# Performance work log

Hardware: AMD Instinct MI355X
Metric: run time of the kernel (lower is better)

Reference implementation:

```python
import jax, jax.numpy as jnp
import numpy as np

B, S, D_IN = 4, 2048, 512
H, D_OUT = 8, 64


def setup_inputs() -> dict:
    key = jax.random.key(0)
    k1, k2, k3 = jax.random.split(key, 3)
    x = jax.random.normal(k1, (B, S, D_IN), dtype=jnp.float32)
    # matches torch init: w ~ U(-0.8, 0.8), wo ~ U(-1, 1)
    w = jax.random.uniform(k2, (H, 3, D_IN, D_OUT), dtype=jnp.float32, minval=-0.8, maxval=0.8)
    wo = jax.random.uniform(k3, (H * D_OUT, D_OUT), dtype=jnp.float32, minval=-1.0, maxval=1.0)
    return {"x": x, "w": w, "wo": wo}


def reference(x, w, wo):
    d_out = w.shape[-1]
    # batched per-head projections: [B, H, S, D_OUT]
    q = jnp.einsum('bsi,hio->bhso', x, w[:, 0])
    k = jnp.einsum('bsi,hio->bhso', x, w[:, 1])
    v = jnp.einsum('bsi,hio->bhso', x, w[:, 2])
    scores = jnp.einsum('bhso,bhto->bhst', q, k) / jnp.sqrt(jnp.asarray(d_out, x.dtype))
    attn = jax.nn.softmax(scores, axis=-1)
    o = jnp.einsum('bhst,bhto->bhso', attn, v)  # [B, H, S, D_OUT]
    # concat heads along feature dim (head order matches torch cat order)
    o = jnp.transpose(o, (0, 2, 1, 3)).reshape(x.shape[0], x.shape[1], -1)
    return jnp.matmul(o, wo)
```

## Files before the change

### kernel.cpp

```cpp
#include <hip/hip_runtime.h>
#include <cstdint>
#include <cstddef>

#define S_LEN 2048
#define DIN   512
#define DOUT  64
#define NB    4
#define NH    8

typedef __attribute__((ext_vector_type(8))) short bf16x8;
typedef __attribute__((ext_vector_type(8))) _Float16 f16x8;
typedef __attribute__((ext_vector_type(4))) float f32x4;
typedef __attribute__((ext_vector_type(16))) float f32x16;

static __device__ __forceinline__ f32x4 mfma16(bf16x8 a, bf16x8 b, f32x4 c) {
    return __builtin_amdgcn_mfma_f32_16x16x32_bf16(a, b, c, 0, 0, 0);
}
static __device__ __forceinline__ f32x16 mfma32h(f16x8 a, f16x8 b, f32x16 c) {
    return __builtin_amdgcn_mfma_f32_32x32x16_f16(a, b, c, 0, 0, 0);
}

static __device__ __forceinline__ uint16_t f2bf(float x) {
    uint32_t u = __builtin_bit_cast(uint32_t, x);
    u += 0x7fffu + ((u >> 16) & 1u);
    return (uint16_t)(u >> 16);
}
static __device__ __forceinline__ float bf2f(uint16_t h) {
    uint32_t u = ((uint32_t)h) << 16;
    return __builtin_bit_cast(float, u);
}
static __device__ __forceinline__ uint32_t cvt_pk_bf16(float lo, float hi) {
    uint32_t r;
    asm("v_cvt_pk_bf16_f32 %0, %1, %2" : "=v"(r) : "v"(lo), "v"(hi));
    return r;
}
static __device__ __forceinline__ uint32_t cvt_pkrtz_f16(float lo, float hi) {
    return __builtin_bit_cast(uint32_t, __builtin_amdgcn_cvt_pkrtz(lo, hi));
}

typedef const __attribute__((address_space(1))) void* as1p;
typedef __attribute__((address_space(3))) void* as3p;
static __device__ __forceinline__ void gload_lds16(const void* g, void* l) {
    __builtin_amdgcn_global_load_lds((as1p)g, (as3p)l, 16, 0, 0);
}

__global__ __launch_bounds__(256) void prep_w(
    const float* __restrict__ w, const float* __restrict__ wo,
    uint16_t* __restrict__ whiT, uint16_t* __restrict__ wloT,
    uint16_t* __restrict__ woT)
{
    __shared__ float tile[64][65];
    const int blk = blockIdx.x;
    const int t = threadIdx.x;
    const int tq = t >> 6, tr = t & 63;

    if (blk < 192) {
        const int hp = blk >> 3, i0 = (blk & 7) * 64;
        const int p = hp % 3;
        const float s = (p == 0) ? 0.18033688011112042f : 1.0f;
        const float* __restrict__ src = w + (size_t)hp * (DIN * DOUT);
        #pragma unroll
        for (int r = 0; r < 16; ++r) {
            const int ir = r * 4 + tq;
            tile[ir][tr] = src[(size_t)(i0 + ir) * DOUT + tr];
        }
        __syncthreads();
        uint16_t* __restrict__ dh = whiT + (size_t)hp * (DOUT * DIN);
        uint16_t* __restrict__ dl = wloT + (size_t)hp * (DOUT * DIN);
        #pragma unroll
        for (int r = 0; r < 16; ++r) {
            const int o = r * 4 + tq;
            const float v = tile[tr][o] * s;
            const uint16_t hi = f2bf(v);
            dh[(size_t)o * DIN + i0 + tr] = hi;
            dl[(size_t)o * DIN + i0 + tr] = f2bf(v - bf2f(hi));
        }
    } else {
        const int i0 = (blk - 192) * 64;
        #pragma unroll
        for (int r = 0; r < 16; ++r) {
            const int ir = r * 4 + tq;
            tile[ir][tr] = wo[(size_t)(i0 + ir) * DOUT + tr];
        }
        __syncthreads();
        #pragma unroll
        for (int r = 0; r < 16; ++r) {
            const int o = r * 4 + tq;
            woT[(size_t)o * DIN + i0 + tr] = f2bf(tile[tr][o]);
        }
    }
}

__global__ __launch_bounds__(256) void split_x(
    const float* __restrict__ x, uint16_t* __restrict__ xhi, uint16_t* __restrict__ xlo)
{
    const size_t idx = ((size_t)blockIdx.x * 256 + threadIdx.x) * 8;
    const float4 a = *(const float4*)(x + idx);
    const float4 b = *(const float4*)(x + idx + 4);
    const float xv[8] = {a.x, a.y, a.z, a.w, b.x, b.y, b.z, b.w};
    union { uint16_t u[8]; uint4 v; } H, L;
    #pragma unroll
    for (int j = 0; j < 8; ++j) {
        const uint16_t hi = f2bf(xv[j]);
        H.u[j] = hi;
        L.u[j] = f2bf(xv[j] - bf2f(hi));
    }
    *(uint4*)(xhi + idx) = H.v;
    *(uint4*)(xlo + idx) = L.v;
}

__global__ __launch_bounds__(256, 2) void gemm_qkv(
    const uint16_t* __restrict__ xhi, const uint16_t* __restrict__ xlo,
    const uint16_t* __restrict__ whiT, const uint16_t* __restrict__ wloT,
    uint16_t* __restrict__ qf, uint16_t* __restrict__ kf,
    uint16_t* __restrict__ vT)
{
    __shared__ __align__(16) uint16_t lds[4 * 128 * 64];

    const int bid = blockIdx.x;
    const int xcd = bid & 7, wi = bid >> 3;
    const int mt = xcd * 8 + wi / 12, nt = wi % 12;
    const int m0 = mt * 128, n0 = nt * 128;
    const int tid = threadIdx.x;
    const int l = tid & 63, w = tid >> 6;
    const int g = l >> 4, lm = l & 15;
    const int wm = w >> 1, wn = w & 1;

    const f32x4 Z = {0.f, 0.f, 0.f, 0.f};
    f32x4 acc[4][4];
    #pragma unroll
    for (int a = 0; a < 4; ++a)
        #pragma unroll
        for (int b = 0; b < 4; ++b) acc[a][b] = Z;

    int srow[4], scol[4];
    #pragma unroll
    for (int i = 0; i < 4; ++i) {
        const int c = i * 256 + tid;
        srow[i] = c >> 3;
        scol[i] = ((c & 7) * 8) ^ ((srow[i] & 7) << 3);
    }

    for (int kt = 0; kt < 8; ++kt) {
        const int k0 = kt * 64;
        #pragma unroll
        for (int i = 0; i < 4; ++i) {
            const int c8 = (i * 256 + tid) * 8;
            const size_t aoff = (size_t)(m0 + srow[i]) * DIN + k0 + scol[i];
            const size_t boff = (size_t)(n0 + srow[i]) * DIN + k0 + scol[i];
            gload_lds16(xhi  + aoff, &lds[c8]);
            gload_lds16(xlo  + aoff, &lds[128 * 64 + c8]);
            gload_lds16(whiT + boff, &lds[2 * 128 * 64 + c8]);
            gload_lds16(wloT + boff, &lds[3 * 128 * 64 + c8]);
        }
        asm volatile("s_waitcnt vmcnt(0)" ::: "memory");
        __syncthreads();

        bf16x8 ah[4][2], al[4][2];
        #pragma unroll
        for (int mi = 0; mi < 4; ++mi) {
            const int r = wm * 64 + mi * 16 + lm;
            const int rb = r * 128;
            #pragma unroll
            for (int kk = 0; kk < 2; ++kk) {
                const int cb = (kk * 64 + g * 16) ^ ((r & 7) << 4);
                ah[mi][kk] = *(const bf16x8*)((const char*)lds + rb + cb);
                al[mi][kk] = *(const bf16x8*)((const char*)lds + 16384 + rb + cb);
            }
        }
        #pragma unroll
        for (int ni = 0; ni < 4; ++ni) {
            const int r = wn * 64 + ni * 16 + lm;
            const int rb = r * 128;
            bf16x8 bh[2], bl[2];
            #pragma unroll
            for (int kk = 0; kk < 2; ++kk) {
                const int cb = (kk * 64 + g * 16) ^ ((r & 7) << 4);
                bh[kk] = *(const bf16x8*)((const char*)lds + 32768 + rb + cb);
                bl[kk] = *(const bf16x8*)((const char*)lds + 49152 + rb + cb);
            }
            #pragma unroll
            for (int mi = 0; mi < 4; ++mi) {
                acc[mi][ni] = mfma16(ah[mi][0], bh[0], acc[mi][ni]);
                acc[mi][ni] = mfma16(ah[mi][1], bh[1], acc[mi][ni]);
                acc[mi][ni] = mfma16(ah[mi][0], bl[0], acc[mi][ni]);
                acc[mi][ni] = mfma16(ah[mi][1], bl[1], acc[mi][ni]);
                acc[mi][ni] = mfma16(al[mi][0], bh[0], acc[mi][ni]);
                acc[mi][ni] = mfma16(al[mi][1], bh[1], acc[mi][ni]);
            }
        }
        __syncthreads();
    }

    #pragma unroll
    for (int ni = 0; ni < 4; ++ni) {
        const int n = n0 + wn * 64 + ni * 16 + lm;
        const int hp = n >> 6, o = n & 63;
        const int h = hp / 3, p = hp - h * 3;
        if (p < 2) {
            uint16_t* __restrict__ dst = (p == 0) ? qf : kf;
            #pragma unroll
            for (int mi = 0; mi < 4; ++mi) {
                #pragma unroll
                for (int j = 0; j < 4; ++j) {
                    const int m = m0 + wm * 64 + mi * 16 + 4 * g + j;
                    const int b = m >> 11, s = m & 2047;
                    const size_t idx = ((size_t)(b * NH + h) * S_LEN + s) * DOUT + o;
                    const _Float16 hv = (_Float16)acc[mi][ni][j];
                    dst[idx] = __builtin_bit_cast(uint16_t, hv);
                }
            }
        } else {
            #pragma unroll
            for (int mi = 0; mi < 4; ++mi) {
                const int m = m0 + wm * 64 + mi * 16 + 4 * g;
                const int b = m >> 11, s = m & 2047;
                union { _Float16 h[4]; uint2 u; } pk;
                pk.h[0] = (_Float16)acc[mi][ni][0];
                pk.h[1] = (_Float16)acc[mi][ni][1];
                pk.h[2] = (_Float16)acc[mi][ni][2];
                pk.h[3] = (_Float16)acc[mi][ni][3];
                *(uint2*)(vT + ((size_t)((b * NH + h) * DOUT + o)) * S_LEN + s) = pk.u;
            }
        }
    }
}

__global__ __launch_bounds__(256, 2) void attn_fwd(
    const uint16_t* __restrict__ qf, const uint16_t* __restrict__ kf,
    const uint16_t* __restrict__ vT, uint16_t* __restrict__ oc)
{
    __shared__ __align__(16) char smem[32768];
    char* __restrict__ vbufs = smem + 16384;

    const int bid = blockIdx.x;
    const int qt = (bid >> 3) & 15, bh = (bid & 7) + 8 * (bid >> 7);
    const int tid = threadIdx.x;
    const int l = tid & 63, wq = tid >> 6;
    const int L = l >> 5, lq = l & 31;
    const size_t base = (size_t)bh * (S_LEN * DOUT);

    const int c0 = tid, c1 = tid + 256;
    const int kr0 = c0 & 31,        do0 = ((c0 >> 5) & 7) << 3;
    const int kr1 = 32 + (c1 & 31), do1 = ((c1 >> 5) & 7) << 3;

    const int qrow = qt * 128 + wq * 32 + lq;
    const uint16_t* qp = qf + base + (size_t)qrow * DOUT;
    f16x8 qv[4];
    #pragma unroll
    for (int dsub = 0; dsub < 4; ++dsub)
        qv[dsub] = *(const f16x8*)(qp + dsub * 16 + L * 8);

    f32x16 Zv;
    #pragma unroll
    for (int r = 0; r < 16; ++r) Zv[r] = 0.f;
    f32x16 Oa[2] = {Zv, Zv};
    float m_run = -INFINITY, l_run = 0.f;

    auto qk_step = [&](const char* kb2, f32x16* dst) {
        #pragma unroll
        for (int ks = 0; ks < 2; ++ks) {
            f32x16 s = Zv;
            #pragma unroll
            for (int dsub = 0; dsub < 4; ++dsub) {
                const uint32_t off = (uint32_t)(((ks * 4 + dsub) << 10) + (l << 4));
                const f16x8 kfr = *(const f16x8*)(kb2 + off);
                s = mfma32h(kfr, qv[dsub], s);
            }
            dst[ks] = s;
        }
    };

    gload_lds16(kf + base + (size_t)kr0 * DOUT + do0, smem + c0 * 16);
    gload_lds16(kf + base + (size_t)kr1 * DOUT + do1, smem + c1 * 16);
    gload_lds16(kf + base + (size_t)(64 + kr0) * DOUT + do0, smem + 8192 + c0 * 16);
    gload_lds16(kf + base + (size_t)(64 + kr1) * DOUT + do1, smem + 8192 + c1 * 16);
    gload_lds16(vT + base + (size_t)kr0 * S_LEN + do0, vbufs + c0 * 16);
    gload_lds16(vT + base + (size_t)kr1 * S_LEN + do1, vbufs + c1 * 16);
    asm volatile("s_waitcnt vmcnt(0)" ::: "memory");
    __builtin_amdgcn_s_barrier();
    __builtin_amdgcn_sched_barrier(0);

    f32x16 saA[2], saB[2];
    qk_step(smem, saA);

    auto iter = [&](int kt, f32x16* sa, f32x16* sb) {
        asm volatile("s_waitcnt vmcnt(0)" ::: "memory");
        __builtin_amdgcn_s_barrier();
        __builtin_amdgcn_sched_barrier(0);

        {
            char* __restrict__ kn = smem + (kt & 1) * 8192;
            const int sK = (kt < 30) ? (kt + 2) * 64 : 0;
            gload_lds16(kf + base + (size_t)(sK + kr0) * DOUT + do0, kn + c0 * 16);
            gload_lds16(kf + base + (size_t)(sK + kr1) * DOUT + do1, kn + c1 * 16);
            char* __restrict__ vn = vbufs + ((kt + 1) & 1) * 8192;
            const int sV = (kt < 31) ? (kt + 1) * 64 : 0;
            gload_lds16(vT + base + (size_t)kr0 * S_LEN + sV + do0, vn + c0 * 16);
            gload_lds16(vT + base + (size_t)kr1 * S_LEN + sV + do1, vn + c1 * 16);
        }

        qk_step(smem + ((kt + 1) & 1) * 8192, sb);

        float mx[16];
        #pragma unroll
        for (int r = 0; r < 16; ++r) mx[r] = fmaxf(sa[0][r], sa[1][r]);
        #pragma unroll
        for (int st = 8; st >= 1; st >>= 1)
            #pragma unroll
            for (int r = 0; r < st; ++r) mx[r] = fmaxf(mx[r], mx[r + st]);
        float pmax = mx[0];
        pmax = fmaxf(pmax, __shfl_xor(pmax, 32));

        if (!__all(pmax - m_run <= 8.f)) {
            const float m_new = fmaxf(m_run, pmax);
            const float alpha = __builtin_amdgcn_exp2f(m_run - m_new);
            m_run = m_new;
            #pragma unroll
            for (int r = 0; r < 16; ++r) { Oa[0][r] *= alpha; Oa[1][r] *= alpha; }
            l_run *= alpha;
        }

        #pragma unroll
        for (int ks = 0; ks < 2; ++ks)
            #pragma unroll
            for (int r = 0; r < 16; ++r)
                sa[ks][r] = __builtin_amdgcn_exp2f(sa[ks][r] - m_run);

        float sm[16];
        #pragma unroll
        for (int r = 0; r < 16; ++r) sm[r] = sa[0][r] + sa[1][r];
        #pragma unroll
        for (int st = 8; st >= 1; st >>= 1)
            #pragma unroll
            for (int r = 0; r < st; ++r) sm[r] += sm[r + st];
        float lsum = sm[0];
        lsum += __shfl_xor(lsum, 32);
        l_run += lsum;

        f16x8 pfrag[4];
        #pragma unroll
        for (int ks = 0; ks < 2; ++ks) {
            uint32_t a0 = cvt_pkrtz_f16(sa[ks][0], sa[ks][1]);
            uint32_t a1 = cvt_pkrtz_f16(sa[ks][2], sa[ks][3]);
            uint32_t a2 = cvt_pkrtz_f16(sa[ks][4], sa[ks][5]);
            uint32_t a3 = cvt_pkrtz_f16(sa[ks][6], sa[ks][7]);
            asm volatile("v_permlane32_swap_b32 %0, %1" : "+v"(a0), "+v"(a2));
            asm volatile("v_permlane32_swap_b32 %0, %1" : "+v"(a1), "+v"(a3));
            union { uint32_t w[4]; f16x8 v; } u;
            u.w[0] = a0; u.w[1] = a1; u.w[2] = a2; u.w[3] = a3;
            pfrag[2 * ks] = u.v;
            uint32_t b0 = cvt_pkrtz_f16(sa[ks][8],  sa[ks][9]);
            uint32_t b1 = cvt_pkrtz_f16(sa[ks][10], sa[ks][11]);
            uint32_t b2 = cvt_pkrtz_f16(sa[ks][12], sa[ks][13]);
            uint32_t b3 = cvt_pkrtz_f16(sa[ks][14], sa[ks][15]);
            asm volatile("v_permlane32_swap_b32 %0, %1" : "+v"(b0), "+v"(b2));
            asm volatile("v_permlane32_swap_b32 %0, %1" : "+v"(b1), "+v"(b3));
            union { uint32_t w[4]; f16x8 v; } u2;
            u2.w[0] = b0; u2.w[1] = b1; u2.w[2] = b2; u2.w[3] = b3;
            pfrag[2 * ks + 1] = u2.v;
        }

        const char* __restrict__ vb = vbufs + (kt & 1) * 8192;
        __builtin_amdgcn_s_setprio(1);
        #pragma unroll
        for (int dh = 0; dh < 2; ++dh) {
            #pragma unroll
            for (int kc = 0; kc < 4; ++kc) {
                const uint32_t off = (uint32_t)(((dh * 4 + kc) << 10) + (l << 4));
                const f16x8 vv = *(const f16x8*)(vb + off);
                Oa[dh] = mfma32h(vv, pfrag[kc], Oa[dh]);
            }
        }
        __builtin_amdgcn_s_setprio(0);
    };

    for (int kt2 = 0; kt2 < 16; ++kt2) {
        iter(2 * kt2,     saA, saB);
        iter(2 * kt2 + 1, saB, saA);
    }
    asm volatile("s_waitcnt vmcnt(0)" ::: "memory");

    const int b = bh >> 3, hh = bh & 7;
    const float li = 1.f / l_run;
    const int srow = qt * 128 + wq * 32 + lq;
    const size_t rbase = ((size_t)b * S_LEN + srow) * (NH * DOUT) + hh * DOUT;
    #pragma unroll
    for (int dh = 0; dh < 2; ++dh) {
        #pragma unroll
        for (int rq = 0; rq < 4; ++rq) {
            const int d0 = dh * 32 + rq * 8 + L * 4;
            uint2 val;
            val.x = cvt_pk_bf16(Oa[dh][rq * 4 + 0] * li, Oa[dh][rq * 4 + 1] * li);
            val.y = cvt_pk_bf16(Oa[dh][rq * 4 + 2] * li, Oa[dh][rq * 4 + 3] * li);
            *(uint2*)(oc + rbase + d0) = val;
        }
    }
}

__global__ __launch_bounds__(256) void oproj(
    const uint16_t* __restrict__ oc, const uint16_t* __restrict__ woT,
    float* __restrict__ out)
{
    const int mt = blockIdx.x;
    const int tid = threadIdx.x;
    const int l = tid & 63, w = tid >> 6;
    const int g = l >> 4, lm = l & 15;
    const int m0 = mt * 64 + w * 16;
    const f32x4 Z = {0.f, 0.f, 0.f, 0.f};
    f32x4 acc[4] = {Z, Z, Z, Z};
    const uint16_t* __restrict__ arow = oc + (size_t)(m0 + lm) * (NH * DOUT);
    for (int kc = 0; kc < 16; ++kc) {
        const bf16x8 a = *(const bf16x8*)(arow + kc * 32 + g * 8);
        #pragma unroll
        for (int nt = 0; nt < 4; ++nt) {
            const bf16x8 bfr = *(const bf16x8*)(woT + (size_t)(nt * 16 + lm) * (NH * DOUT) + kc * 32 + g * 8);
            acc[nt] = mfma16(a, bfr, acc[nt]);
        }
    }
    #pragma unroll
    for (int nt = 0; nt < 4; ++nt)
        #pragma unroll
        for (int j = 0; j < 4; ++j)
            out[(size_t)(m0 + 4 * g + j) * DOUT + nt * 16 + lm] = acc[nt][j];
}

extern "C" void kernel_launch(void* const* d_in, const int* in_sizes, int n_in,
                              void* d_out, int out_size, void* d_ws, size_t ws_size,
                              hipStream_t stream) {
    const float* x  = (const float*)d_in[0];
    const float* w  = (const float*)d_in[1];
    const float* wo = (const float*)d_in[2];
    float* out = (float*)d_out;

    char* ws = (char*)d_ws;
    uint16_t* qf   = (uint16_t*)(ws);
    uint16_t* kf   = (uint16_t*)(ws + 8388608);
    uint16_t* vT   = (uint16_t*)(ws + 16777216);
    uint16_t* xhi  = (uint16_t*)(ws + 25165824);
    uint16_t* xlo  = (uint16_t*)(ws + 33554432);
    uint16_t* whiT = (uint16_t*)(ws + 41943040);
    uint16_t* wloT = (uint16_t*)(ws + 43515904);
    uint16_t* woT  = (uint16_t*)(ws + 45088768);
    uint16_t* oc   = xhi;

    hipLaunchKernelGGL(prep_w, dim3(200), dim3(256), 0, stream, w, wo, whiT, wloT, woT);
    hipLaunchKernelGGL(split_x, dim3(2048), dim3(256), 0, stream, x, xhi, xlo);
    hipLaunchKernelGGL(gemm_qkv, dim3(768), dim3(256), 0, stream,
                       xhi, xlo, whiT, wloT, qf, kf, vT);
    hipLaunchKernelGGL(attn_fwd, dim3(512), dim3(256), 0, stream,
                       qf, kf, vT, oc);
    hipLaunchKernelGGL(oproj, dim3(128), dim3(256), 0, stream, oc, woT, out);
}
```

Before: 114.3 us.

## Split attention over two KV halves and merge partial outputs

Splits the attention forward pass along the key/value sequence into two halves, doubling the grid from 512 to 1024 blocks. Each block writes unnormalized-then-normalized fp16 partial outputs plus per-row max and sum. A new merge kernel combines the two halves with log-sum-exp weighting and writes the bf16 concatenated output for the projection. This is meant to improve occupancy and load balance across the CUs, at the cost of an extra kernel launch and extra global traffic for the partials.

After: 120.8 us. 5.7% more time.

```diff
diff --git a/kernel.cpp b/kernel.cpp
--- a/kernel.cpp
+++ b/kernel.cpp
@@ -228,13 +228,16 @@
 
 __global__ __launch_bounds__(256, 2) void attn_fwd(
     const uint16_t* __restrict__ qf, const uint16_t* __restrict__ kf,
-    const uint16_t* __restrict__ vT, uint16_t* __restrict__ oc)
+    const uint16_t* __restrict__ vT,
+    uint16_t* __restrict__ part0, uint16_t* __restrict__ part1,
+    float2* __restrict__ ml)
 {
     __shared__ __align__(16) char smem[32768];
     char* __restrict__ vbufs = smem + 16384;
 
     const int bid = blockIdx.x;
-    const int qt = (bid >> 3) & 15, bh = (bid & 7) + 8 * (bid >> 7);
+    const int half = bid >> 9, qt = (bid >> 5) & 15, bh = bid & 31;
+    const int sbase = half * 1024;
     const int tid = threadIdx.x;
     const int l = tid & 63, wq = tid >> 6;
     const int L = l >> 5, lq = l & 31;
@@ -271,12 +274,12 @@
         }
     };
 
-    gload_lds16(kf + base + (size_t)kr0 * DOUT + do0, smem + c0 * 16);
-    gload_lds16(kf + base + (size_t)kr1 * DOUT + do1, smem + c1 * 16);
-    gload_lds16(kf + base + (size_t)(64 + kr0) * DOUT + do0, smem + 8192 + c0 * 16);
-    gload_lds16(kf + base + (size_t)(64 + kr1) * DOUT + do1, smem + 8192 + c1 * 16);
-    gload_lds16(vT + base + (size_t)kr0 * S_LEN + do0, vbufs + c0 * 16);
-    gload_lds16(vT + base + (size_t)kr1 * S_LEN + do1, vbufs + c1 * 16);
+    gload_lds16(kf + base + (size_t)(sbase + kr0) * DOUT + do0, smem + c0 * 16);
+    gload_lds16(kf + base + (size_t)(sbase + kr1) * DOUT + do1, smem + c1 * 16);
+    gload_lds16(kf + base + (size_t)(sbase + 64 + kr0) * DOUT + do0, smem + 8192 + c0 * 16);
+    gload_lds16(kf + base + (size_t)(sbase + 64 + kr1) * DOUT + do1, smem + 8192 + c1 * 16);
+    gload_lds16(vT + base + (size_t)kr0 * S_LEN + sbase + do0, vbufs + c0 * 16);
+    gload_lds16(vT + base + (size_t)kr1 * S_LEN + sbase + do1, vbufs + c1 * 16);
     asm volatile("s_waitcnt vmcnt(0)" ::: "memory");
     __builtin_amdgcn_s_barrier();
     __builtin_amdgcn_sched_barrier(0);
@@ -291,11 +294,11 @@
 
         {
             char* __restrict__ kn = smem + (kt & 1) * 8192;
-            const int sK = (kt < 30) ? (kt + 2) * 64 : 0;
+            const int sK = sbase + ((kt < 14) ? (kt + 2) * 64 : 0);
             gload_lds16(kf + base + (size_t)(sK + kr0) * DOUT + do0, kn + c0 * 16);
             gload_lds16(kf + base + (size_t)(sK + kr1) * DOUT + do1, kn + c1 * 16);
             char* __restrict__ vn = vbufs + ((kt + 1) & 1) * 8192;
-            const int sV = (kt < 31) ? (kt + 1) * 64 : 0;
+            const int sV = sbase + ((kt < 15) ? (kt + 1) * 64 : 0);
             gload_lds16(vT + base + (size_t)kr0 * S_LEN + sV + do0, vn + c0 * 16);
             gload_lds16(vT + base + (size_t)kr1 * S_LEN + sV + do1, vn + c1 * 16);
         }
@@ -375,27 +378,62 @@
         __builtin_amdgcn_s_setprio(0);
     };
 
-    for (int kt2 = 0; kt2 < 16; ++kt2) {
+    for (int kt2 = 0; kt2 < 8; ++kt2) {
         iter(2 * kt2,     saA, saB);
         iter(2 * kt2 + 1, saB, saA);
     }
     asm volatile("s_waitcnt vmcnt(0)" ::: "memory");
 
-    const int b = bh >> 3, hh = bh & 7;
+    uint16_t* __restrict__ pd = half ? part1 : part0;
     const float li = 1.f / l_run;
     const int srow = qt * 128 + wq * 32 + lq;
-    const size_t rbase = ((size_t)b * S_LEN + srow) * (NH * DOUT) + hh * DOUT;
+    const size_t rbase = ((size_t)bh * S_LEN + srow) * DOUT;
     #pragma unroll
     for (int dh = 0; dh < 2; ++dh) {
         #pragma unroll
         for (int rq = 0; rq < 4; ++rq) {
             const int d0 = dh * 32 + rq * 8 + L * 4;
             uint2 val;
-            val.x = cvt_pk_bf16(Oa[dh][rq * 4 + 0] * li, Oa[dh][rq * 4 + 1] * li);
-            val.y = cvt_pk_bf16(Oa[dh][rq * 4 + 2] * li, Oa[dh][rq * 4 + 3] * li);
-            *(uint2*)(oc + rbase + d0) = val;
-        }
-    }
+            val.x = cvt_pkrtz_f16(Oa[dh][rq * 4 + 0] * li, Oa[dh][rq * 4 + 1] * li);
+            val.y = cvt_pkrtz_f16(Oa[dh][rq * 4 + 2] * li, Oa[dh][rq * 4 + 3] * li);
+            *(uint2*)(pd + rbase + d0) = val;
+        }
+    }
+    if (L == 0) {
+        float2 v; v.x = m_run; v.y = l_run;
+        ml[((size_t)half << 16) | ((size_t)bh << 11) | (size_t)srow] = v;
+    }
+}
+
+__global__ __launch_bounds__(256) void merge_o(
+    const uint16_t* __restrict__ part0, const uint16_t* __restrict__ part1,
+    const float2* __restrict__ ml, uint16_t* __restrict__ oc)
+{
+    const int g = blockIdx.x * 256 + threadIdx.x;
+    const int row = g >> 3, dp = (g & 7) * 8;
+    const int bh = row >> 11, s = row & 2047;
+
+    const float2 ml0 = ml[row];
+    const float2 ml1 = ml[65536 + row];
+    const float m = fmaxf(ml0.x, ml1.x);
+    float w0 = ml0.y * __builtin_amdgcn_exp2f(ml0.x - m);
+    float w1 = ml1.y * __builtin_amdgcn_exp2f(ml1.x - m);
+    const float inv = 1.f / (w0 + w1);
+    w0 *= inv; w1 *= inv;
+
+    const size_t poff = (size_t)row * 64 + dp;
+    union { uint4 u; f16x8 v; } a, b;
+    a.u = *(const uint4*)(part0 + poff);
+    b.u = *(const uint4*)(part1 + poff);
+    union { uint32_t w[4]; uint4 u; } r;
+    #pragma unroll
+    for (int j = 0; j < 4; ++j) {
+        const float o0 = w0 * (float)a.v[2 * j]     + w1 * (float)b.v[2 * j];
+        const float o1 = w0 * (float)a.v[2 * j + 1] + w1 * (float)b.v[2 * j + 1];
+        r.w[j] = cvt_pk_bf16(o0, o1);
+    }
+    const int bb = bh >> 3, h = bh & 7;
+    *(uint4*)(oc + ((size_t)(bb * S_LEN + s) * (NH * DOUT)) + h * DOUT + dp) = r.u;
 }
 
 __global__ __launch_bounds__(256) void oproj(
@@ -434,21 +472,26 @@
     float* out = (float*)d_out;
 
     char* ws = (char*)d_ws;
-    uint16_t* qf   = (uint16_t*)(ws);
-    uint16_t* kf   = (uint16_t*)(ws + 8388608);
-    uint16_t* vT   = (uint16_t*)(ws + 16777216);
-    uint16_t* xhi  = (uint16_t*)(ws + 25165824);
-    uint16_t* xlo  = (uint16_t*)(ws + 33554432);
-    uint16_t* whiT = (uint16_t*)(ws + 41943040);
-    uint16_t* wloT = (uint16_t*)(ws + 43515904);
-    uint16_t* woT  = (uint16_t*)(ws + 45088768);
-    uint16_t* oc   = xhi;
+    uint16_t* qf    = (uint16_t*)(ws);
+    uint16_t* kf    = (uint16_t*)(ws + 8388608);
+    uint16_t* vT    = (uint16_t*)(ws + 16777216);
+    uint16_t* xhi   = (uint16_t*)(ws + 25165824);
+    uint16_t* xlo   = (uint16_t*)(ws + 33554432);
+    uint16_t* part1 = (uint16_t*)(ws + 41943040);
+    float2*   ml    = (float2*)  (ws + 50331648);
+    uint16_t* whiT  = (uint16_t*)(ws + 51380224);
+    uint16_t* wloT  = (uint16_t*)(ws + 52953088);
+    uint16_t* woT   = (uint16_t*)(ws + 54525952);
+    uint16_t* oc    = xhi;
+    uint16_t* part0 = xlo;
 
     hipLaunchKernelGGL(prep_w, dim3(200), dim3(256), 0, stream, w, wo, whiT, wloT, woT);
     hipLaunchKernelGGL(split_x, dim3(2048), dim3(256), 0, stream, x, xhi, xlo);
     hipLaunchKernelGGL(gemm_qkv, dim3(768), dim3(256), 0, stream,
                        xhi, xlo, whiT, wloT, qf, kf, vT);
-    hipLaunchKernelGGL(attn_fwd, dim3(512), dim3(256), 0, stream,
-                       qf, kf, vT, oc);
+    hipLaunchKernelGGL(attn_fwd, dim3(1024), dim3(256), 0, stream,
+                       qf, kf, vT, part0, part1, ml);
+    hipLaunchKernelGGL(merge_o, dim3(2048), dim3(256), 0, stream,
+                       part0, part1, ml, oc);
     hipLaunchKernelGGL(oproj, dim3(128), dim3(256), 0, stream, oc, woT, out);
 }
```

## Load attention K/V fragments straight to registers and stage GEMM through VGPRs

Applied to the files above, without the earlier changes.

The attention kernel drops its LDS double buffers and barriers. Each wave loads its own K and V MFMA fragments from global memory into registers, software-pipelined one tile ahead, and the per-iteration row-sum shuffle is deferred to the end. The projection GEMM replaces direct global-to-LDS loads with register-staged loads followed by LDS stores. This removes barrier synchronisation and LDS traffic, at the cost of more VGPR pressure and redundant global/L2 reads across the four waves that share K/V.

New measurement: 186.1 us. 62.8% more time.

```diff
diff --git a/kernel.cpp b/kernel.cpp
--- a/kernel.cpp
+++ b/kernel.cpp
@@ -36,12 +36,6 @@
 }
 static __device__ __forceinline__ uint32_t cvt_pkrtz_f16(float lo, float hi) {
     return __builtin_bit_cast(uint32_t, __builtin_amdgcn_cvt_pkrtz(lo, hi));
-}
-
-typedef const __attribute__((address_space(1))) void* as1p;
-typedef __attribute__((address_space(3))) void* as3p;
-static __device__ __forceinline__ void gload_lds16(const void* g, void* l) {
-    __builtin_amdgcn_global_load_lds((as1p)g, (as3p)l, 16, 0, 0);
 }
 
 __global__ __launch_bounds__(256) void prep_w(
@@ -143,17 +137,24 @@
 
     for (int kt = 0; kt < 8; ++kt) {
         const int k0 = kt * 64;
+        uint4 stg[16];
+        #pragma unroll
+        for (int i = 0; i < 4; ++i) {
+            const size_t aoff = (size_t)(m0 + srow[i]) * DIN + k0 + scol[i];
+            const size_t boff = (size_t)(n0 + srow[i]) * DIN + k0 + scol[i];
+            stg[i * 4 + 0] = *(const uint4*)(xhi  + aoff);
+            stg[i * 4 + 1] = *(const uint4*)(xlo  + aoff);
+            stg[i * 4 + 2] = *(const uint4*)(whiT + boff);
+            stg[i * 4 + 3] = *(const uint4*)(wloT + boff);
+        }
         #pragma unroll
         for (int i = 0; i < 4; ++i) {
             const int c8 = (i * 256 + tid) * 8;
-            const size_t aoff = (size_t)(m0 + srow[i]) * DIN + k0 + scol[i];
-            const size_t boff = (size_t)(n0 + srow[i]) * DIN + k0 + scol[i];
-            gload_lds16(xhi  + aoff, &lds[c8]);
-            gload_lds16(xlo  + aoff, &lds[128 * 64 + c8]);
-            gload_lds16(whiT + boff, &lds[2 * 128 * 64 + c8]);
-            gload_lds16(wloT + boff, &lds[3 * 128 * 64 + c8]);
-        }
-        asm volatile("s_waitcnt vmcnt(0)" ::: "memory");
+            *(uint4*)&lds[c8]                 = stg[i * 4 + 0];
+            *(uint4*)&lds[128 * 64 + c8]      = stg[i * 4 + 1];
+            *(uint4*)&lds[2 * 128 * 64 + c8]  = stg[i * 4 + 2];
+            *(uint4*)&lds[3 * 128 * 64 + c8]  = stg[i * 4 + 3];
+        }
         __syncthreads();
 
         bf16x8 ah[4][2], al[4][2];
@@ -230,9 +231,6 @@
     const uint16_t* __restrict__ qf, const uint16_t* __restrict__ kf,
     const uint16_t* __restrict__ vT, uint16_t* __restrict__ oc)
 {
-    __shared__ __align__(16) char smem[32768];
-    char* __restrict__ vbufs = smem + 16384;
-
     const int bid = blockIdx.x;
     const int qt = (bid >> 3) & 15, bh = (bid & 7) + 8 * (bid >> 7);
     const int tid = threadIdx.x;
@@ -240,10 +238,6 @@
     const int L = l >> 5, lq = l & 31;
     const size_t base = (size_t)bh * (S_LEN * DOUT);
 
-    const int c0 = tid, c1 = tid + 256;
-    const int kr0 = c0 & 31,        do0 = ((c0 >> 5) & 7) << 3;
-    const int kr1 = 32 + (c1 & 31), do1 = ((c1 >> 5) & 7) << 3;
-
     const int qrow = qt * 128 + wq * 32 + lq;
     const uint16_t* qp = qf + base + (size_t)qrow * DOUT;
     f16x8 qv[4];
@@ -251,56 +245,54 @@
     for (int dsub = 0; dsub < 4; ++dsub)
         qv[dsub] = *(const f16x8*)(qp + dsub * 16 + L * 8);
 
+    const uint16_t* kp = kf + base + (size_t)lq * DOUT + L * 8;
+    const uint16_t* vp = vT + base + (size_t)lq * S_LEN + L * 8;
+
     f32x16 Zv;
     #pragma unroll
     for (int r = 0; r < 16; ++r) Zv[r] = 0.f;
     f32x16 Oa[2] = {Zv, Zv};
     float m_run = -INFINITY, l_run = 0.f;
 
-    auto qk_step = [&](const char* kb2, f32x16* dst) {
+    f16x8 KA[8], KB[8], Vr[8];
+
+    auto loadK = [&](f16x8* dst, int t) {
+        #pragma unroll
+        for (int ks = 0; ks < 2; ++ks)
+            #pragma unroll
+            for (int dsub = 0; dsub < 4; ++dsub)
+                dst[ks * 4 + dsub] =
+                    *(const f16x8*)(kp + t * 4096 + ks * 2048 + dsub * 16);
+    };
+    auto loadV = [&](f16x8* dst, int t) {
+        #pragma unroll
+        for (int dh = 0; dh < 2; ++dh)
+            #pragma unroll
+            for (int kc = 0; kc < 4; ++kc)
+                dst[dh * 4 + kc] =
+                    *(const f16x8*)(vp + dh * 65536 + t * 64 + kc * 16);
+    };
+    auto qk_step = [&](const f16x8* K, f32x16* dst) {
+        __builtin_amdgcn_s_setprio(1);
         #pragma unroll
         for (int ks = 0; ks < 2; ++ks) {
             f32x16 s = Zv;
             #pragma unroll
-            for (int dsub = 0; dsub < 4; ++dsub) {
-                const uint32_t off = (uint32_t)(((ks * 4 + dsub) << 10) + (l << 4));
-                const f16x8 kfr = *(const f16x8*)(kb2 + off);
-                s = mfma32h(kfr, qv[dsub], s);
-            }
+            for (int dsub = 0; dsub < 4; ++dsub)
+                s = mfma32h(K[ks * 4 + dsub], qv[dsub], s);
             dst[ks] = s;
         }
+        __builtin_amdgcn_s_setprio(0);
     };
 
-    gload_lds16(kf + base + (size_t)kr0 * DOUT + do0, smem + c0 * 16);
-    gload_lds16(kf + base + (size_t)kr1 * DOUT + do1, smem + c1 * 16);
-    gload_lds16(kf + base + (size_t)(64 + kr0) * DOUT + do0, smem + 8192 + c0 * 16);
-    gload_lds16(kf + base + (size_t)(64 + kr1) * DOUT + do1, smem + 8192 + c1 * 16);
-    gload_lds16(vT + base + (size_t)kr0 * S_LEN + do0, vbufs + c0 * 16);
-    gload_lds16(vT + base + (size_t)kr1 * S_LEN + do1, vbufs + c1 * 16);
-    asm volatile("s_waitcnt vmcnt(0)" ::: "memory");
-    __builtin_amdgcn_s_barrier();
-    __builtin_amdgcn_sched_barrier(0);
-
+    loadK(KA, 0);
+    loadK(KB, 1);
+    loadV(Vr, 0);
     f32x16 saA[2], saB[2];
-    qk_step(smem, saA);
-
-    auto iter = [&](int kt, f32x16* sa, f32x16* sb) {
-        asm volatile("s_waitcnt vmcnt(0)" ::: "memory");
-        __builtin_amdgcn_s_barrier();
-        __builtin_amdgcn_sched_barrier(0);
-
-        {
-            char* __restrict__ kn = smem + (kt & 1) * 8192;
-            const int sK = (kt < 30) ? (kt + 2) * 64 : 0;
-            gload_lds16(kf + base + (size_t)(sK + kr0) * DOUT + do0, kn + c0 * 16);
-            gload_lds16(kf + base + (size_t)(sK + kr1) * DOUT + do1, kn + c1 * 16);
-            char* __restrict__ vn = vbufs + ((kt + 1) & 1) * 8192;
-            const int sV = (kt < 31) ? (kt + 1) * 64 : 0;
-            gload_lds16(vT + base + (size_t)kr0 * S_LEN + sV + do0, vn + c0 * 16);
-            gload_lds16(vT + base + (size_t)kr1 * S_LEN + sV + do1, vn + c1 * 16);
-        }
-
-        qk_step(smem + ((kt + 1) & 1) * 8192, sb);
+    qk_step(KA, saA);
+
+    auto body = [&](int kt, f32x16* sa, f32x16* sb, const f16x8* Kuse) {
+        qk_step(Kuse, sb);
 
         float mx[16];
         #pragma unroll
@@ -309,11 +301,11 @@
         for (int st = 8; st >= 1; st >>= 1)
             #pragma unroll
             for (int r = 0; r < st; ++r) mx[r] = fmaxf(mx[r], mx[r + st]);
-        float pmax = mx[0];
-        pmax = fmaxf(pmax, __shfl_xor(pmax, 32));
+        const float pmax = mx[0];
 
         if (!__all(pmax - m_run <= 8.f)) {
-            const float m_new = fmaxf(m_run, pmax);
+            const float pmr = fmaxf(pmax, __shfl_xor(pmax, 32));
+            const float m_new = fmaxf(m_run, pmr);
             const float alpha = __builtin_amdgcn_exp2f(m_run - m_new);
             m_run = m_new;
             #pragma unroll
@@ -334,9 +326,7 @@
         for (int st = 8; st >= 1; st >>= 1)
             #pragma unroll
             for (int r = 0; r < st; ++r) sm[r] += sm[r + st];
-        float lsum = sm[0];
-        lsum += __shfl_xor(lsum, 32);
-        l_run += lsum;
+        l_run += sm[0];
 
         f16x8 pfrag[4];
         #pragma unroll
@@ -361,28 +351,28 @@
             pfrag[2 * ks + 1] = u2.v;
         }
 
-        const char* __restrict__ vb = vbufs + (kt & 1) * 8192;
         __builtin_amdgcn_s_setprio(1);
         #pragma unroll
-        for (int dh = 0; dh < 2; ++dh) {
-            #pragma unroll
-            for (int kc = 0; kc < 4; ++kc) {
-                const uint32_t off = (uint32_t)(((dh * 4 + kc) << 10) + (l << 4));
-                const f16x8 vv = *(const f16x8*)(vb + off);
-                Oa[dh] = mfma32h(vv, pfrag[kc], Oa[dh]);
-            }
-        }
+        for (int dh = 0; dh < 2; ++dh)
+            #pragma unroll
+            for (int kc = 0; kc < 4; ++kc)
+                Oa[dh] = mfma32h(Vr[dh * 4 + kc], pfrag[kc], Oa[dh]);
         __builtin_amdgcn_s_setprio(0);
+
+        loadV(Vr, (kt + 1 < 32) ? kt + 1 : 0);
     };
 
-    for (int kt2 = 0; kt2 < 16; ++kt2) {
-        iter(2 * kt2,     saA, saB);
-        iter(2 * kt2 + 1, saB, saA);
-    }
-    asm volatile("s_waitcnt vmcnt(0)" ::: "memory");
-
+    for (int t = 0; t < 16; ++t) {
+        const int kt0 = 2 * t, kt1 = 2 * t + 1;
+        loadK(KA, (kt0 + 2 < 32) ? kt0 + 2 : 0);
+        body(kt0, saA, saB, KB);
+        loadK(KB, (kt1 + 2 < 32) ? kt1 + 2 : 0);
+        body(kt1, saB, saA, KA);
+    }
+
+    const float l_row = l_run + __shfl_xor(l_run, 32);
+    const float li = 1.f / l_row;
     const int b = bh >> 3, hh = bh & 7;
-    const float li = 1.f / l_run;
     const int srow = qt * 128 + wq * 32 + lq;
     const size_t rbase = ((size_t)b * S_LEN + srow) * (NH * DOUT) + hh * DOUT;
     #pragma unroll
```

## Replace direct global-to-LDS loads with register-staged prefetch pipelines

Applied to the files above, without the earlier changes.

Both the projection GEMM and the attention kernel stop using global_load_lds and instead load tiles into registers first, then write them to LDS. In attention, K/V tiles are prefetched two iterations ahead into register staging buffers and committed to LDS at the end of each iteration, between two barriers. The LDS tile layout is also changed, and setprio is added around the QK MFMAs. The aim is to hide global-memory latency behind compute, at the cost of more VGPR pressure and an extra barrier per iteration. The GEMM change still waits on its loads within the same iteration, so it gains little overlap there.

Measured after the change: 154.4 us. 35.1% more time.

```diff
diff --git a/kernel.cpp b/kernel.cpp
--- a/kernel.cpp
+++ b/kernel.cpp
@@ -36,12 +36,6 @@
 }
 static __device__ __forceinline__ uint32_t cvt_pkrtz_f16(float lo, float hi) {
     return __builtin_bit_cast(uint32_t, __builtin_amdgcn_cvt_pkrtz(lo, hi));
-}
-
-typedef const __attribute__((address_space(1))) void* as1p;
-typedef __attribute__((address_space(3))) void* as3p;
-static __device__ __forceinline__ void gload_lds16(const void* g, void* l) {
-    __builtin_amdgcn_global_load_lds((as1p)g, (as3p)l, 16, 0, 0);
 }
 
 __global__ __launch_bounds__(256) void prep_w(
@@ -143,17 +137,24 @@
 
     for (int kt = 0; kt < 8; ++kt) {
         const int k0 = kt * 64;
+        uint4 stg[16];
+        #pragma unroll
+        for (int i = 0; i < 4; ++i) {
+            const size_t aoff = (size_t)(m0 + srow[i]) * DIN + k0 + scol[i];
+            const size_t boff = (size_t)(n0 + srow[i]) * DIN + k0 + scol[i];
+            stg[i * 4 + 0] = *(const uint4*)(xhi  + aoff);
+            stg[i * 4 + 1] = *(const uint4*)(xlo  + aoff);
+            stg[i * 4 + 2] = *(const uint4*)(whiT + boff);
+            stg[i * 4 + 3] = *(const uint4*)(wloT + boff);
+        }
         #pragma unroll
         for (int i = 0; i < 4; ++i) {
             const int c8 = (i * 256 + tid) * 8;
-            const size_t aoff = (size_t)(m0 + srow[i]) * DIN + k0 + scol[i];
-            const size_t boff = (size_t)(n0 + srow[i]) * DIN + k0 + scol[i];
-            gload_lds16(xhi  + aoff, &lds[c8]);
-            gload_lds16(xlo  + aoff, &lds[128 * 64 + c8]);
-            gload_lds16(whiT + boff, &lds[2 * 128 * 64 + c8]);
-            gload_lds16(wloT + boff, &lds[3 * 128 * 64 + c8]);
-        }
-        asm volatile("s_waitcnt vmcnt(0)" ::: "memory");
+            *(uint4*)&lds[c8]                 = stg[i * 4 + 0];
+            *(uint4*)&lds[128 * 64 + c8]      = stg[i * 4 + 1];
+            *(uint4*)&lds[2 * 128 * 64 + c8]  = stg[i * 4 + 2];
+            *(uint4*)&lds[3 * 128 * 64 + c8]  = stg[i * 4 + 3];
+        }
         __syncthreads();
 
         bf16x8 ah[4][2], al[4][2];
@@ -240,9 +241,10 @@
     const int L = l >> 5, lq = l & 31;
     const size_t base = (size_t)bh * (S_LEN * DOUT);
 
-    const int c0 = tid, c1 = tid + 256;
-    const int kr0 = c0 & 31,        do0 = ((c0 >> 5) & 7) << 3;
-    const int kr1 = 32 + (c1 & 31), do1 = ((c1 >> 5) & 7) << 3;
+    const int tr = tid >> 3, tc8 = (tid & 7) * 8;
+    const uint16_t* __restrict__ kgb = kf + base + (size_t)tr * DOUT + tc8;
+    const uint16_t* __restrict__ vgb = vT + base + (size_t)tr * S_LEN + tc8;
+    const uint32_t wo16 = (uint32_t)(((tid & 7) * 32 + tr) * 16);
 
     const int qrow = qt * 128 + wq * 32 + lq;
     const uint16_t* qp = qf + base + (size_t)qrow * DOUT;
@@ -257,7 +259,24 @@
     f32x16 Oa[2] = {Zv, Zv};
     float m_run = -INFINITY, l_run = 0.f;
 
+    uint4 stgA[4], stgB[4];
+    auto issue = [&](int tk, uint4* stg) {
+        const int s0 = (tk < 32) ? tk * 64 : 0;
+        stg[0] = *(const uint4*)(kgb + (size_t)s0 * DOUT);
+        stg[1] = *(const uint4*)(kgb + (size_t)(s0 + 32) * DOUT);
+        stg[2] = *(const uint4*)(vgb + s0);
+        stg[3] = *(const uint4*)(vgb + (size_t)32 * S_LEN + s0);
+    };
+    auto commit = [&](int tk, const uint4* stg) {
+        char* __restrict__ kb = smem + (tk & 1) * 8192;
+        char* __restrict__ vb = vbufs + (tk & 1) * 8192;
+        *(uint4*)(kb + wo16)        = stg[0];
+        *(uint4*)(kb + 4096 + wo16) = stg[1];
+        *(uint4*)(vb + wo16)        = stg[2];
+        *(uint4*)(vb + 4096 + wo16) = stg[3];
+    };
     auto qk_step = [&](const char* kb2, f32x16* dst) {
+        __builtin_amdgcn_s_setprio(1);
         #pragma unroll
         for (int ks = 0; ks < 2; ++ks) {
             f32x16 s = Zv;
@@ -269,37 +288,23 @@
             }
             dst[ks] = s;
         }
+        __builtin_amdgcn_s_setprio(0);
     };
 
-    gload_lds16(kf + base + (size_t)kr0 * DOUT + do0, smem + c0 * 16);
-    gload_lds16(kf + base + (size_t)kr1 * DOUT + do1, smem + c1 * 16);
-    gload_lds16(kf + base + (size_t)(64 + kr0) * DOUT + do0, smem + 8192 + c0 * 16);
-    gload_lds16(kf + base + (size_t)(64 + kr1) * DOUT + do1, smem + 8192 + c1 * 16);
-    gload_lds16(vT + base + (size_t)kr0 * S_LEN + do0, vbufs + c0 * 16);
-    gload_lds16(vT + base + (size_t)kr1 * S_LEN + do1, vbufs + c1 * 16);
-    asm volatile("s_waitcnt vmcnt(0)" ::: "memory");
+    issue(0, stgA);
+    issue(1, stgB);
+    commit(0, stgA);
+    commit(1, stgB);
+    issue(2, stgA);
+    issue(3, stgB);
+    asm volatile("s_waitcnt lgkmcnt(0)" ::: "memory");
     __builtin_amdgcn_s_barrier();
     __builtin_amdgcn_sched_barrier(0);
 
     f32x16 saA[2], saB[2];
     qk_step(smem, saA);
 
-    auto iter = [&](int kt, f32x16* sa, f32x16* sb) {
-        asm volatile("s_waitcnt vmcnt(0)" ::: "memory");
-        __builtin_amdgcn_s_barrier();
-        __builtin_amdgcn_sched_barrier(0);
-
-        {
-            char* __restrict__ kn = smem + (kt & 1) * 8192;
-            const int sK = (kt < 30) ? (kt + 2) * 64 : 0;
-            gload_lds16(kf + base + (size_t)(sK + kr0) * DOUT + do0, kn + c0 * 16);
-            gload_lds16(kf + base + (size_t)(sK + kr1) * DOUT + do1, kn + c1 * 16);
-            char* __restrict__ vn = vbufs + ((kt + 1) & 1) * 8192;
-            const int sV = (kt < 31) ? (kt + 1) * 64 : 0;
-            gload_lds16(vT + base + (size_t)kr0 * S_LEN + sV + do0, vn + c0 * 16);
-            gload_lds16(vT + base + (size_t)kr1 * S_LEN + sV + do1, vn + c1 * 16);
-        }
-
+    auto iter = [&](int kt, f32x16* sa, f32x16* sb, uint4* stg) {
         qk_step(smem + ((kt + 1) & 1) * 8192, sb);
 
         float mx[16];
@@ -373,13 +378,19 @@
             }
         }
         __builtin_amdgcn_s_setprio(0);
+
+        __builtin_amdgcn_s_barrier();
+        commit(kt + 2, stg);
+        issue(kt + 4, stg);
+        asm volatile("s_waitcnt lgkmcnt(0)" ::: "memory");
+        __builtin_amdgcn_sched_barrier(0);
+        __builtin_amdgcn_s_barrier();
     };
 
-    for (int kt2 = 0; kt2 < 16; ++kt2) {
-        iter(2 * kt2,     saA, saB);
-        iter(2 * kt2 + 1, saB, saA);
-    }
-    asm volatile("s_waitcnt vmcnt(0)" ::: "memory");
+    for (int t = 0; t < 16; ++t) {
+        iter(2 * t,     saA, saB, stgA);
+        iter(2 * t + 1, saB, saA, stgB);
+    }
 
     const int b = bh >> 3, hh = bh & 7;
     const float li = 1.f / l_run;
```
